# Kernel optimization log

Measured on AMD Instinct MI355X. Metric: run time of the kernel, lower is better.

The kernel has to match this reference:

```python
import jax, jax.numpy as jnp
import numpy as np

B, C, H, W = 64, 512, 32, 32
R = 32  # reduction_channels = max(512 // 16, 8)


def setup_inputs() -> dict:
    key = jax.random.key(0)
    ks = jax.random.split(key, 10)
    s = 0.05
    return {
        "x": jax.random.normal(ks[0], (B, C, H, W), jnp.float32),
        "w_fc1": jax.random.normal(ks[1], (R, C), jnp.float32) * s,
        "b_fc1": jax.random.normal(ks[2], (R,), jnp.float32) * s,
        "w_fc2": jax.random.normal(ks[3], (C, R), jnp.float32) * s,
        "b_fc2": jax.random.normal(ks[4], (C,), jnp.float32) * s,
        "w_eig": jax.random.normal(ks[5], (R, C), jnp.float32) * s,
        "b_eig": jax.random.normal(ks[6], (R,), jnp.float32) * s,
        "w_sp": jax.random.normal(ks[7], (C,), jnp.float32) * s,
        "b_sp": jax.random.normal(ks[8], (1,), jnp.float32) * s,
        # random init vector for power iteration (torch.randn in the module)
        "v0": jax.random.normal(ks[9], (B, R, 1), jnp.float32),
    }


def reference(x, w_fc1, b_fc1, w_fc2, b_fc2, w_eig, b_eig, w_sp, b_sp, v0):
    b, c, h, w = x.shape
    hw = h * w

    # ---- channel attention (SE): global avg pool -> fc1 -> relu -> fc2 -> sigmoid
    pooled = jnp.mean(x, axis=(2, 3))                     # [B, C]
    ca = jax.nn.relu(jnp.einsum("bc,rc->br", pooled, w_fc1) + b_fc1)
    ca = jax.nn.sigmoid(jnp.einsum("br,cr->bc", ca, w_fc2) + b_fc2)
    channel_att = ca[:, :, None, None]                    # [B, C, 1, 1]

    # ---- eigen attention branch
    feat = jnp.einsum("bchw,rc->brhw", x, w_eig) + b_eig[None, :, None, None]
    feat = feat.reshape(b, R, hw)                         # [B, R, HW]
    feat_c = feat - jnp.mean(feat, axis=2, keepdims=True)
    cov = jnp.einsum("brn,bsn->brs", feat_c, feat_c) / (hw - 1)
    cov = cov + 1e-5 * jnp.eye(R, dtype=x.dtype)

    v = v0 / jnp.linalg.norm(v0, axis=1, keepdims=True)
    for _ in range(5):  # 5-step power iteration
        v = jnp.einsum("brs,bsi->bri", cov, v)
        v = v / (jnp.linalg.norm(v, axis=1, keepdims=True) + 1e-10)

    att = jnp.einsum("bri,brn->bn", v, feat_c).reshape(b, 1, h, w)
    amin = jnp.min(att, axis=(2, 3), keepdims=True)
    att = att - amin
    amax = jnp.max(att, axis=(2, 3), keepdims=True)
    eigen_att = jax.nn.sigmoid(att / (amax + 1e-10))      # [B, 1, H, W]

    # ---- spatial attention: 1x1 conv C->1 -> sigmoid
    spatial_att = jax.nn.sigmoid(
        jnp.einsum("bchw,c->bhw", x, w_sp)[:, None] + b_sp[0]
    )                                                      # [B, 1, H, W]

    att_all = eigen_att * spatial_att
    return x * channel_att * att_all + x
```

## Files before the change

### kernel.cpp

```cpp
#include <hip/hip_runtime.h>
#include <hip/hip_bf16.h>

#define B_ 64
#define C_ 512
#define HW_ 1024
#define R_ 32
#define NCHUNK 4
#define CPB 128
#define Q_ 4
#define PPB 256

__device__ __forceinline__ float dpp_fold8(float s) {
    int y;
    y = __builtin_amdgcn_update_dpp(0, __float_as_int(s), 0xB1, 0xF, 0xF, true);
    s += __int_as_float(y);
    y = __builtin_amdgcn_update_dpp(0, __float_as_int(s), 0x4E, 0xF, 0xF, true);
    s += __int_as_float(y);
    y = __builtin_amdgcn_update_dpp(0, __float_as_int(s), 0x141, 0xF, 0xF, true);
    s += __int_as_float(y);
    return s;
}

__global__ void k_transpose_w(const float* __restrict__ w_eig,
                              float* __restrict__ wt) {
    int idx = blockIdx.x * 1024 + threadIdx.x;
    int r = idx >> 9;
    int c = idx & 511;
    wt[c * R_ + r] = w_eig[idx];
}

__global__ __launch_bounds__(256, 4) void k_proj(
    const float* __restrict__ x, const float* __restrict__ wt,
    const float* __restrict__ w_sp,
    __hip_bfloat16* __restrict__ featp, __hip_bfloat16* __restrict__ sppb,
    float* __restrict__ pooledp)
{
    const int t   = threadIdx.x;
    const int blk = blockIdx.x;
    const int q   = blk & 3;
    const int ch  = (blk >> 2) & 3;
    const int b   = blk >> 4;
    const int c0  = ch * CPB;
    const int n   = q * PPB + t;

    __shared__ float plds[CPB][33];
    __shared__ float red2[CPB][2];

    const float* wch = wt + (size_t)c0 * R_;

    float acc[R_];
#pragma unroll
    for (int r = 0; r < R_; ++r) acc[r] = 0.f;
    float sp = 0.f;

    const float* xb = x + ((size_t)(b * C_ + c0)) * HW_ + n;

    float xv = xb[0];
#pragma unroll 2
    for (int j = 0; j < CPB; ++j) {
        float xn = xb[(size_t)((j + 1) & (CPB - 1)) * HW_];

        const float4* wr = (const float4*)(wch + j * R_);
#pragma unroll
        for (int k = 0; k < 8; ++k) {
            float4 w = wr[k];
            acc[4 * k + 0] = fmaf(w.x, xv, acc[4 * k + 0]);
            acc[4 * k + 1] = fmaf(w.y, xv, acc[4 * k + 1]);
            acc[4 * k + 2] = fmaf(w.z, xv, acc[4 * k + 2]);
            acc[4 * k + 3] = fmaf(w.w, xv, acc[4 * k + 3]);
        }

        sp = fmaf(w_sp[c0 + j], xv, sp);

        float s = dpp_fold8(xv);
        if ((t & 7) == 0) plds[j][t >> 3] = s;

        xv = xn;
    }
    __syncthreads();

    {
        const int j = t >> 1, h = t & 1;
        float s = 0.f;
#pragma unroll
        for (int i = 0; i < 16; ++i) s += plds[j][h * 16 + i];
        red2[j][h] = s;
    }
    __syncthreads();
    if (t < CPB)
        pooledp[(((size_t)q * B_ + b) * C_) + c0 + t] = red2[t][0] + red2[t][1];

    sppb[((size_t)(ch * B_ + b)) * HW_ + n] = __float2bfloat16(sp);

    __hip_bfloat16* fb = featp + ((size_t)((ch * B_ + b) * HW_ + n)) * R_;
    union { __hip_bfloat16 h[R_]; uint4 qv[4]; } u;
#pragma unroll
    for (int r = 0; r < R_; ++r) u.h[r] = __float2bfloat16(acc[r]);
#pragma unroll
    for (int k = 0; k < 4; ++k) ((uint4*)fb)[k] = u.qv[k];
}

__global__ __launch_bounds__(1024) void k_eigen(
    const __hip_bfloat16* __restrict__ featp,
    const __hip_bfloat16* __restrict__ sppb,
    const float* __restrict__ pooledp,
    const float* __restrict__ w_eig, const float* __restrict__ w_fc1,
    const float* __restrict__ b_fc1, const float* __restrict__ w_fc2,
    const float* __restrict__ b_fc2, const float* __restrict__ b_sp,
    const float* __restrict__ v0,
    float* __restrict__ ca_out, float* __restrict__ att_out)
{
    const int b    = blockIdx.x;
    const int t    = threadIdx.x;
    const int lane = t & 63;
    const int wave = t >> 6;

    __shared__ float pooledm[C_];
    __shared__ float meanv[R_], t1[R_], vv[R_], wred[R_];
    __shared__ float plds2[R_ / 2][128][2];
    __shared__ float redmn[16], redmx[16], scal[2];

    if (t < C_) {
        float s = 0.f;
#pragma unroll
        for (int qq = 0; qq < Q_; ++qq)
            s += pooledp[((size_t)qq * B_ + b) * C_ + t];
        pooledm[t] = s * (1.f / 1024.f);
    }
    __syncthreads();

    if (t < 512) {
        const int r = t >> 4, k = t & 15;
        float pm = 0.f, pf = 0.f;
        for (int c = k; c < C_; c += 16) {
            float p = pooledm[c];
            pm = fmaf(w_eig[r * C_ + c], p, pm);
            pf = fmaf(w_fc1[r * C_ + c], p, pf);
        }
#pragma unroll
        for (int m = 8; m > 0; m >>= 1) {
            pm += __shfl_xor(pm, m, 64);
            pf += __shfl_xor(pf, m, 64);
        }
        if (k == 0) { meanv[r] = pm; t1[r] = fmaxf(pf + b_fc1[r], 0.f); }
    }
    __syncthreads();

    if (t < C_) {
        float s = b_fc2[t];
        const float4* w4 = (const float4*)(w_fc2 + (size_t)t * R_);
#pragma unroll
        for (int k = 0; k < 8; ++k) {
            float4 w = w4[k];
            s = fmaf(w.x, t1[4 * k + 0], s);
            s = fmaf(w.y, t1[4 * k + 1], s);
            s = fmaf(w.z, t1[4 * k + 2], s);
            s = fmaf(w.w, t1[4 * k + 3], s);
        }
        ca_out[b * C_ + t] = 1.f / (1.f + expf(-s));
    }

    float col[R_];
#pragma unroll
    for (int r = 0; r < R_; ++r) col[r] = -meanv[r];
    for (int ch = 0; ch < NCHUNK; ++ch) {
        union { __hip_bfloat16 h[R_]; uint4 qv[4]; } u;
        const uint4* src =
            (const uint4*)(featp + ((size_t)((ch * B_ + b) * HW_ + t)) * R_);
#pragma unroll
        for (int k = 0; k < 4; ++k) u.qv[k] = src[k];
#pragma unroll
        for (int r = 0; r < R_; ++r) col[r] += __bfloat162float(u.h[r]);
    }

    if (t < 64) {
        float vl = (t < R_) ? v0[b * R_ + t] : 0.f;
        float sq = vl * vl;
#pragma unroll
        for (int m = 32; m > 0; m >>= 1) sq += __shfl_xor(sq, m, 64);
        if (t < R_) vv[t] = vl / sqrtf(sq);
    }
    __syncthreads();

    for (int it = 0; it < 5; ++it) {
        float uacc = 0.f;
#pragma unroll
        for (int r = 0; r < R_; ++r) uacc = fmaf(col[r], vv[r], uacc);
        uacc *= (1.f / 1023.f);

#pragma unroll
        for (int g = 0; g < R_ / 2; ++g) {
            float s0 = dpp_fold8(col[2 * g + 0] * uacc);
            float s1 = dpp_fold8(col[2 * g + 1] * uacc);
            if ((t & 7) == 0) {
                plds2[g][t >> 3][0] = s0;
                plds2[g][t >> 3][1] = s1;
            }
        }
        __syncthreads();

        {
            const int r = t >> 5, i = t & 31;
            const int g = r >> 1, e = r & 1;
            float s = plds2[g][i][e] + plds2[g][i + 32][e] +
                      plds2[g][i + 64][e] + plds2[g][i + 96][e];
#pragma unroll
            for (int m = 16; m > 0; m >>= 1) s += __shfl_xor(s, m, 64);
            if (i == 0) wred[r] = s;
        }
        __syncthreads();

        if (t < 64) {
            float w = (t < R_) ? wred[t] + 1e-5f * vv[t] : 0.f;
            float sq = w * w;
#pragma unroll
            for (int m = 32; m > 0; m >>= 1) sq += __shfl_xor(sq, m, 64);
            if (t < R_) vv[t] = w / (sqrtf(sq) + 1e-10f);
        }
        __syncthreads();
    }

    float a = 0.f;
#pragma unroll
    for (int r = 0; r < R_; ++r) a = fmaf(col[r], vv[r], a);

    float mn = a, mx = a;
#pragma unroll
    for (int m = 32; m > 0; m >>= 1) {
        mn = fminf(mn, __shfl_xor(mn, m, 64));
        mx = fmaxf(mx, __shfl_xor(mx, m, 64));
    }
    if (lane == 0) { redmn[wave] = mn; redmx[wave] = mx; }
    __syncthreads();
    if (t == 0) {
        float m1 = redmn[0], m2 = redmx[0];
        for (int w = 1; w < 16; ++w) {
            m1 = fminf(m1, redmn[w]);
            m2 = fmaxf(m2, redmx[w]);
        }
        scal[0] = m1; scal[1] = m2;
    }
    __syncthreads();

    const float amin  = scal[0];
    const float denom = (scal[1] - scal[0]) + 1e-10f;
    float eig = 1.f / (1.f + expf(-((a - amin) / denom)));

    float ssum = b_sp[0];
#pragma unroll
    for (int ch = 0; ch < NCHUNK; ++ch)
        ssum += __bfloat162float(sppb[((size_t)(ch * B_ + b)) * HW_ + t]);
    float spsig = 1.f / (1.f + expf(-ssum));

    att_out[b * HW_ + t] = eig * spsig;
}

__global__ __launch_bounds__(256) void k_final(
    const float* __restrict__ x, const float* __restrict__ ca,
    const float* __restrict__ att, float* __restrict__ out)
{
    const int t   = threadIdx.x;
    const int blk = blockIdx.x;
    const int b   = blk >> 9;
    const float cav  = ca[blk];
    const size_t base = (size_t)blk * HW_;

    float4 xv = ((const float4*)(x + base))[t];
    float4 av = ((const float4*)(att + (size_t)b * HW_))[t];
    float4 o;
    o.x = fmaf(xv.x * cav, av.x, xv.x);
    o.y = fmaf(xv.y * cav, av.y, xv.y);
    o.z = fmaf(xv.z * cav, av.z, xv.z);
    o.w = fmaf(xv.w * cav, av.w, xv.w);
    ((float4*)(out + base))[t] = o;
}

extern "C" void kernel_launch(void* const* d_in, const int* in_sizes, int n_in,
                              void* d_out, int out_size, void* d_ws, size_t ws_size,
                              hipStream_t stream) {
    const float* x     = (const float*)d_in[0];
    const float* w_fc1 = (const float*)d_in[1];
    const float* b_fc1 = (const float*)d_in[2];
    const float* w_fc2 = (const float*)d_in[3];
    const float* b_fc2 = (const float*)d_in[4];
    const float* w_eig = (const float*)d_in[5];
    const float* w_sp  = (const float*)d_in[7];
    const float* b_sp  = (const float*)d_in[8];
    const float* v0    = (const float*)d_in[9];
    float* out = (float*)d_out;

    char* ws = (char*)d_ws;
    __hip_bfloat16* featp = (__hip_bfloat16*)ws;
    __hip_bfloat16* sppb  = (__hip_bfloat16*)(ws + 16777216);
    float* pooledp = (float*)(ws + 17301504);
    float* ca      = (float*)(ws + 17825792);
    float* att     = (float*)(ws + 17956864);
    float* wt      = (float*)(ws + 18219008);

    k_transpose_w<<<16, 1024, 0, stream>>>(w_eig, wt);
    k_proj<<<B_ * NCHUNK * Q_, 256, 0, stream>>>(x, wt, w_sp,
                                                 featp, sppb, pooledp);
    k_eigen<<<B_, 1024, 0, stream>>>(featp, sppb, pooledp, w_eig, w_fc1, b_fc1,
                                     w_fc2, b_fc2, b_sp, v0, ca, att);
    k_final<<<B_ * C_, 256, 0, stream>>>(x, ca, att, out);
}
```

Baseline: 117.3 us.

## Compute eigen and spatial projections with bf16 MFMA over all channels per block

Replaces the scalar FMA projection kernel with one that packs w_eig and w_sp into MFMA fragments in a prep kernel, converts x to bf16 on the fly, and runs 16x16x32 bf16 MFMAs across all 512 channels per pixel group. Because each block now covers every channel, the per-chunk partial feature and spatial buffers are gone, which cuts workspace writes and the reduction reads in k_eigen. The spatial term comes out of a third padded MFMA and is stored as fp32. The cost is quantizing x and the weights to bf16 before accumulation, plus 16 pooled partials per batch instead of 4.

```diff
diff --git a/kernel.cpp b/kernel.cpp
--- a/kernel.cpp
+++ b/kernel.cpp
@@ -5,10 +5,129 @@
 #define C_ 512
 #define HW_ 1024
 #define R_ 32
-#define NCHUNK 4
-#define CPB 128
-#define Q_ 4
-#define PPB 256
+#define NPXG 16
+
+typedef __attribute__((ext_vector_type(8))) short bf16x8;
+typedef __attribute__((ext_vector_type(4))) float f32x4;
+
+union U8 { uint4 q; bf16x8 v; unsigned short s[8]; };
+
+__device__ __forceinline__ unsigned short f2bf(float f) {
+    __hip_bfloat16 h = __float2bfloat16(f);
+    union { __hip_bfloat16 b; unsigned short u; } c; c.b = h; return c.u;
+}
+
+__device__ __forceinline__ float dpp_fold16(float s) {
+    int y;
+    y = __builtin_amdgcn_update_dpp(0, __float_as_int(s), 0xB1, 0xF, 0xF, true);
+    s += __int_as_float(y);
+    y = __builtin_amdgcn_update_dpp(0, __float_as_int(s), 0x4E, 0xF, 0xF, true);
+    s += __int_as_float(y);
+    y = __builtin_amdgcn_update_dpp(0, __float_as_int(s), 0x141, 0xF, 0xF, true);
+    s += __int_as_float(y);
+    y = __builtin_amdgcn_update_dpp(0, __float_as_int(s), 0x140, 0xF, 0xF, true);
+    s += __int_as_float(y);
+    return s;
+}
+
+__global__ void k_prep(const float* __restrict__ w_eig,
+                       const float* __restrict__ w_sp,
+                       uint4* __restrict__ wfrag) {
+    int idx   = blockIdx.x * 256 + threadIdx.x;
+    int lane  = idx & 63;
+    int kstep = (idx >> 6) & 15;
+    int slot  = idx >> 10;
+    int m = lane & 15, g = lane >> 4;
+    int cbase = kstep * 32 + 8 * g;
+
+    U8 u;
+    if (slot < 2) {
+        int r = slot * 16 + m;
+#pragma unroll
+        for (int i = 0; i < 8; ++i) u.s[i] = f2bf(w_eig[r * C_ + cbase + i]);
+    } else {
+#pragma unroll
+        for (int i = 0; i < 8; ++i)
+            u.s[i] = (m == 0) ? f2bf(w_sp[cbase + i]) : (unsigned short)0;
+    }
+    wfrag[idx] = u.q;
+}
+
+__global__ __launch_bounds__(256, 4) void k_proj(
+    const float* __restrict__ x, const uint4* __restrict__ wfrag,
+    __hip_bfloat16* __restrict__ featp, float* __restrict__ spp,
+    float* __restrict__ pooledp)
+{
+    const int t    = threadIdx.x;
+    const int lane = t & 63;
+    const int wv   = t >> 6;
+    const int blk  = blockIdx.x;
+    const int b    = blk >> 4;
+    const int pxg  = blk & 15;
+    const int px0  = pxg * 64 + wv * 16;
+    const int g    = lane >> 4;
+    const int col  = lane & 15;
+    const int px   = px0 + col;
+
+    __shared__ float plds[C_][5];
+
+    f32x4 acc0 = {0.f, 0.f, 0.f, 0.f};
+    f32x4 acc1 = {0.f, 0.f, 0.f, 0.f};
+    f32x4 acc2 = {0.f, 0.f, 0.f, 0.f};
+
+    const float* xb = x + (size_t)b * C_ * HW_ + px;
+    const uint4* wf = wfrag + lane;
+
+    for (int ks = 0; ks < 16; ++ks) {
+        const int c8 = ks * 32 + 8 * g;
+        const float* xc = xb + (size_t)c8 * HW_;
+
+        float x0 = xc[0 * HW_], x1 = xc[1 * HW_], x2 = xc[2 * HW_],
+              x3 = xc[3 * HW_], x4 = xc[4 * HW_], x5 = xc[5 * HW_],
+              x6 = xc[6 * HW_], x7 = xc[7 * HW_];
+
+        U8 a0, a1, a2, bu;
+        a0.q = wf[(0 * 16 + ks) * 64];
+        a1.q = wf[(1 * 16 + ks) * 64];
+        a2.q = wf[(2 * 16 + ks) * 64];
+        bu.s[0] = f2bf(x0); bu.s[1] = f2bf(x1);
+        bu.s[2] = f2bf(x2); bu.s[3] = f2bf(x3);
+        bu.s[4] = f2bf(x4); bu.s[5] = f2bf(x5);
+        bu.s[6] = f2bf(x6); bu.s[7] = f2bf(x7);
+
+        acc0 = __builtin_amdgcn_mfma_f32_16x16x32_bf16(a0.v, bu.v, acc0, 0, 0, 0);
+        acc1 = __builtin_amdgcn_mfma_f32_16x16x32_bf16(a1.v, bu.v, acc1, 0, 0, 0);
+        acc2 = __builtin_amdgcn_mfma_f32_16x16x32_bf16(a2.v, bu.v, acc2, 0, 0, 0);
+
+        float s0 = dpp_fold16(x0), s1 = dpp_fold16(x1);
+        float s2 = dpp_fold16(x2), s3 = dpp_fold16(x3);
+        float s4 = dpp_fold16(x4), s5 = dpp_fold16(x5);
+        float s6 = dpp_fold16(x6), s7 = dpp_fold16(x7);
+        if (col == 0) {
+            plds[c8 + 0][wv] = s0; plds[c8 + 1][wv] = s1;
+            plds[c8 + 2][wv] = s2; plds[c8 + 3][wv] = s3;
+            plds[c8 + 4][wv] = s4; plds[c8 + 5][wv] = s5;
+            plds[c8 + 6][wv] = s6; plds[c8 + 7][wv] = s7;
+        }
+    }
+
+    if (lane < 16) spp[(size_t)b * HW_ + px0 + lane] = acc2.x;
+
+    __hip_bfloat16* fb = featp + ((size_t)b * HW_ + px) * R_;
+    ushort4 p0, p1;
+    p0.x = f2bf(acc0.x); p0.y = f2bf(acc0.y);
+    p0.z = f2bf(acc0.z); p0.w = f2bf(acc0.w);
+    p1.x = f2bf(acc1.x); p1.y = f2bf(acc1.y);
+    p1.z = f2bf(acc1.z); p1.w = f2bf(acc1.w);
+    *(ushort4*)(fb + 4 * g)      = p0;
+    *(ushort4*)(fb + 16 + 4 * g) = p1;
+
+    __syncthreads();
+    for (int c = t; c < C_; c += 256) {
+        float s = plds[c][0] + plds[c][1] + plds[c][2] + plds[c][3];
+        pooledp[((size_t)pxg * B_ + b) * C_ + c] = s;
+    }
+}
 
 __device__ __forceinline__ float dpp_fold8(float s) {
     int y;
@@ -21,88 +140,8 @@
     return s;
 }
 
-__global__ void k_transpose_w(const float* __restrict__ w_eig,
-                              float* __restrict__ wt) {
-    int idx = blockIdx.x * 1024 + threadIdx.x;
-    int r = idx >> 9;
-    int c = idx & 511;
-    wt[c * R_ + r] = w_eig[idx];
-}
-
-__global__ __launch_bounds__(256, 4) void k_proj(
-    const float* __restrict__ x, const float* __restrict__ wt,
-    const float* __restrict__ w_sp,
-    __hip_bfloat16* __restrict__ featp, __hip_bfloat16* __restrict__ sppb,
-    float* __restrict__ pooledp)
-{
-    const int t   = threadIdx.x;
-    const int blk = blockIdx.x;
-    const int q   = blk & 3;
-    const int ch  = (blk >> 2) & 3;
-    const int b   = blk >> 4;
-    const int c0  = ch * CPB;
-    const int n   = q * PPB + t;
-
-    __shared__ float plds[CPB][33];
-    __shared__ float red2[CPB][2];
-
-    const float* wch = wt + (size_t)c0 * R_;
-
-    float acc[R_];
-#pragma unroll
-    for (int r = 0; r < R_; ++r) acc[r] = 0.f;
-    float sp = 0.f;
-
-    const float* xb = x + ((size_t)(b * C_ + c0)) * HW_ + n;
-
-    float xv = xb[0];
-#pragma unroll 2
-    for (int j = 0; j < CPB; ++j) {
-        float xn = xb[(size_t)((j + 1) & (CPB - 1)) * HW_];
-
-        const float4* wr = (const float4*)(wch + j * R_);
-#pragma unroll
-        for (int k = 0; k < 8; ++k) {
-            float4 w = wr[k];
-            acc[4 * k + 0] = fmaf(w.x, xv, acc[4 * k + 0]);
-            acc[4 * k + 1] = fmaf(w.y, xv, acc[4 * k + 1]);
-            acc[4 * k + 2] = fmaf(w.z, xv, acc[4 * k + 2]);
-            acc[4 * k + 3] = fmaf(w.w, xv, acc[4 * k + 3]);
-        }
-
-        sp = fmaf(w_sp[c0 + j], xv, sp);
-
-        float s = dpp_fold8(xv);
-        if ((t & 7) == 0) plds[j][t >> 3] = s;
-
-        xv = xn;
-    }
-    __syncthreads();
-
-    {
-        const int j = t >> 1, h = t & 1;
-        float s = 0.f;
-#pragma unroll
-        for (int i = 0; i < 16; ++i) s += plds[j][h * 16 + i];
-        red2[j][h] = s;
-    }
-    __syncthreads();
-    if (t < CPB)
-        pooledp[(((size_t)q * B_ + b) * C_) + c0 + t] = red2[t][0] + red2[t][1];
-
-    sppb[((size_t)(ch * B_ + b)) * HW_ + n] = __float2bfloat16(sp);
-
-    __hip_bfloat16* fb = featp + ((size_t)((ch * B_ + b) * HW_ + n)) * R_;
-    union { __hip_bfloat16 h[R_]; uint4 qv[4]; } u;
-#pragma unroll
-    for (int r = 0; r < R_; ++r) u.h[r] = __float2bfloat16(acc[r]);
-#pragma unroll
-    for (int k = 0; k < 4; ++k) ((uint4*)fb)[k] = u.qv[k];
-}
-
 __global__ __launch_bounds__(1024) void k_eigen(
-    const __hip_bfloat16* __restrict__ featp,
-    const __hip_bfloat16* __restrict__ sppb,
+    const __hip_bfloat16* __restrict__ featp, const float* __restrict__ spp,
     const float* __restrict__ pooledp,
     const float* __restrict__ w_eig, const float* __restrict__ w_fc1,
     const float* __restrict__ b_fc1, const float* __restrict__ w_fc2,
@@ -123,8 +162,8 @@
     if (t < C_) {
         float s = 0.f;
 #pragma unroll
-        for (int qq = 0; qq < Q_; ++qq)
-            s += pooledp[((size_t)qq * B_ + b) * C_ + t];
+        for (int pg = 0; pg < NPXG; ++pg)
+            s += pooledp[((size_t)pg * B_ + b) * C_ + t];
         pooledm[t] = s * (1.f / 1024.f);
     }
     __syncthreads();
@@ -161,16 +200,14 @@
     }
 
     float col[R_];
-#pragma unroll
-    for (int r = 0; r < R_; ++r) col[r] = -meanv[r];
-    for (int ch = 0; ch < NCHUNK; ++ch) {
+    {
         union { __hip_bfloat16 h[R_]; uint4 qv[4]; } u;
-        const uint4* src =
-            (const uint4*)(featp + ((size_t)((ch * B_ + b) * HW_ + t)) * R_);
+        const uint4* src = (const uint4*)(featp + ((size_t)b * HW_ + t) * R_);
 #pragma unroll
         for (int k = 0; k < 4; ++k) u.qv[k] = src[k];
 #pragma unroll
-        for (int r = 0; r < R_; ++r) col[r] += __bfloat162float(u.h[r]);
+        for (int r = 0; r < R_; ++r)
+            col[r] = __bfloat162float(u.h[r]) - meanv[r];
     }
 
     if (t < 64) {
@@ -189,21 +226,21 @@
         uacc *= (1.f / 1023.f);
 
 #pragma unroll
-        for (int g = 0; g < R_ / 2; ++g) {
-            float s0 = dpp_fold8(col[2 * g + 0] * uacc);
-            float s1 = dpp_fold8(col[2 * g + 1] * uacc);
+        for (int gg = 0; gg < R_ / 2; ++gg) {
+            float s0 = dpp_fold8(col[2 * gg + 0] * uacc);
+            float s1 = dpp_fold8(col[2 * gg + 1] * uacc);
             if ((t & 7) == 0) {
-                plds2[g][t >> 3][0] = s0;
-                plds2[g][t >> 3][1] = s1;
+                plds2[gg][t >> 3][0] = s0;
+                plds2[gg][t >> 3][1] = s1;
             }
         }
         __syncthreads();
 
         {
             const int r = t >> 5, i = t & 31;
-            const int g = r >> 1, e = r & 1;
-            float s = plds2[g][i][e] + plds2[g][i + 32][e] +
-                      plds2[g][i + 64][e] + plds2[g][i + 96][e];
+            const int gg = r >> 1, e = r & 1;
+            float s = plds2[gg][i][e] + plds2[gg][i + 32][e] +
+                      plds2[gg][i + 64][e] + plds2[gg][i + 96][e];
 #pragma unroll
             for (int m = 16; m > 0; m >>= 1) s += __shfl_xor(s, m, 64);
             if (i == 0) wred[r] = s;
@@ -246,11 +283,7 @@
     const float denom = (scal[1] - scal[0]) + 1e-10f;
     float eig = 1.f / (1.f + expf(-((a - amin) / denom)));
 
-    float ssum = b_sp[0];
-#pragma unroll
-    for (int ch = 0; ch < NCHUNK; ++ch)
-        ssum += __bfloat162float(sppb[((size_t)(ch * B_ + b)) * HW_ + t]);
-    float spsig = 1.f / (1.f + expf(-ssum));
+    float spsig = 1.f / (1.f + expf(-(b_sp[0] + spp[(size_t)b * HW_ + t])));
 
     att_out[b * HW_ + t] = eig * spsig;
 }
@@ -291,16 +324,15 @@
 
     char* ws = (char*)d_ws;
     __hip_bfloat16* featp = (__hip_bfloat16*)ws;
-    __hip_bfloat16* sppb  = (__hip_bfloat16*)(ws + 16777216);
-    float* pooledp = (float*)(ws + 17301504);
-    float* ca      = (float*)(ws + 17825792);
-    float* att     = (float*)(ws + 17956864);
-    float* wt      = (float*)(ws + 18219008);
-
-    k_transpose_w<<<16, 1024, 0, stream>>>(w_eig, wt);
-    k_proj<<<B_ * NCHUNK * Q_, 256, 0, stream>>>(x, wt, w_sp,
-                                                 featp, sppb, pooledp);
-    k_eigen<<<B_, 1024, 0, stream>>>(featp, sppb, pooledp, w_eig, w_fc1, b_fc1,
+    float* spp     = (float*)(ws + 4194304);
+    float* pooledp = (float*)(ws + 4456448);
+    float* ca      = (float*)(ws + 6553600);
+    float* att     = (float*)(ws + 6684672);
+    uint4* wfrag   = (uint4*)(ws + 6946816);
+
+    k_prep<<<12, 256, 0, stream>>>(w_eig, w_sp, wfrag);
+    k_proj<<<B_ * NPXG, 256, 0, stream>>>(x, wfrag, featp, spp, pooledp);
+    k_eigen<<<B_, 1024, 0, stream>>>(featp, spp, pooledp, w_eig, w_fc1, b_fc1,
                                      w_fc2, b_fc2, b_sp, v0, ca, att);
     k_final<<<B_ * C_, 256, 0, stream>>>(x, ca, att, out);
 }
```

After: 94.83 us, median of 2. 1.24x faster.
